# Performance work log

Measured on AMD Instinct MI355X. Metric: run time of the kernel, lower is better.

## Reference

```python
import jax, jax.numpy as jnp
import numpy as np

B, S, D, H, HS = 2, 2048, 1024, 16, 64


def setup_inputs() -> dict:
    key = jax.random.key(0)
    ks = jax.random.split(key, 4)
    x = jax.random.normal(ks[0], (B, S, D), dtype=jnp.float32)
    # causal mask: 1.0 where key_pos <= query_pos, else 0.0
    mask = jnp.tril(jnp.ones((S, S), dtype=jnp.float32))
    w_qkv = jax.random.normal(ks[1], (D, 3, H, HS), dtype=jnp.float32) * 0.02
    b_qkv = jnp.zeros((3, H, HS), dtype=jnp.float32)
    w_proj = jax.random.normal(ks[2], (H, HS, D), dtype=jnp.float32) * 0.02
    b_proj = jnp.zeros((D,), dtype=jnp.float32)
    return {"x": x, "mask": mask, "w_qkv": w_qkv, "b_qkv": b_qkv,
            "w_proj": w_proj, "b_proj": b_proj}


def reference(x, mask, w_qkv, b_qkv, w_proj, b_proj):
    # c_attn: [B,S,D] @ [D,3,H,HS] -> [B,S,3,H,HS]
    qkv = jnp.einsum('bsd,dthc->bsthc', x, w_qkv) + b_qkv
    q, k, v = qkv[:, :, 0], qkv[:, :, 1], qkv[:, :, 2]  # [B,S,H,HS]
    scale = jax.lax.rsqrt(float(HS))
    q = q * scale
    # scores over head_size: [B,H,S(query),S(key)]
    scores = jnp.einsum('bqhc,bkhc->bhqk', q, k)
    scores = scores + (1.0 - mask) * -1e9
    weights = jax.nn.softmax(scores, axis=-1).astype(x.dtype)
    # attn_pdrop = 0.0 / inference: dropout is identity
    attn = jnp.einsum('bhqk,bkhc->bqhc', weights, v)  # [B,S,H,HS]
    out = jnp.einsum('bqhc,hcd->bqd', attn, w_proj) + b_proj
    return out
```

## Files before the change

### kernel.cpp

```cpp
#include <hip/hip_runtime.h>
#include <hip/hip_bf16.h>


#define Bb 2
#define Ss 2048
#define Dd 1024
#define Hh 16
#define HSs 64

typedef __bf16 bf16x8 __attribute__((ext_vector_type(8)));
typedef float  f32x4  __attribute__((ext_vector_type(4)));

__device__ __forceinline__ unsigned short f2bf(float f) {
  unsigned int u = __float_as_uint(f);
  unsigned int lsb = (u >> 16) & 1u;
  u += 0x7fffu + lsb;
  return (unsigned short)(u >> 16);
}

__device__ __forceinline__ void async16(const unsigned short* g, unsigned short* l) {
  __builtin_amdgcn_global_load_lds(
      (const __attribute__((address_space(1))) unsigned int*)g,
      (__attribute__((address_space(3))) unsigned int*)l,
      16, 0, 0);
}

__global__ __launch_bounds__(256) void k_cvt_bf16(const float* __restrict__ in,
                                                  unsigned short* __restrict__ out,
                                                  int n) {
  int i = (blockIdx.x * 256 + threadIdx.x) * 4;
  int stride = gridDim.x * 256 * 4;
  for (; i < n; i += stride) {
    float4 v = *reinterpret_cast<const float4*>(in + i);
    ushort4 o;
    o.x = f2bf(v.x); o.y = f2bf(v.y); o.z = f2bf(v.z); o.w = f2bf(v.w);
    *reinterpret_cast<ushort4*>(out + i) = o;
  }
}

__global__ __launch_bounds__(256) void k_transpose_bf16(const float* __restrict__ in,
                                                        unsigned short* __restrict__ out,
                                                        int R, int C) {
  __shared__ float t[32][33];
  int c0 = blockIdx.x * 32, r0 = blockIdx.y * 32;
  int tx = threadIdx.x, ty = threadIdx.y;
  #pragma unroll
  for (int i = 0; i < 32; i += 8)
    t[ty + i][tx] = in[(size_t)(r0 + ty + i) * C + (c0 + tx)];
  __syncthreads();
  #pragma unroll
  for (int i = 0; i < 32; i += 8)
    out[(size_t)(c0 + ty + i) * R + (r0 + tx)] = f2bf(t[tx][ty + i]);
}

__global__ __launch_bounds__(256) void k_gemm_qkv(const unsigned short* __restrict__ A,
                                                  const unsigned short* __restrict__ Bt,
                                                  const float* __restrict__ bias,
                                                  unsigned short* __restrict__ Qg,
                                                  unsigned short* __restrict__ Kg,
                                                  unsigned short* __restrict__ Vt) {
  __shared__ unsigned short As[128 * 64];
  __shared__ unsigned short Bs[128 * 64];
  const int K = 1024;
  int bid = blockIdx.x;
  int swz = (bid % 8) * 96 + bid / 8;
  int tm = swz / 24, tn = swz % 24;
  int m0 = tm * 128, n0 = tn * 128;
  int tid = threadIdx.x;
  int w = tid >> 6, l = tid & 63;
  int lr = l & 15, lg = l >> 4;
  int wm = (w >> 1) * 64, wn = (w & 1) * 64;
  int srow = l >> 3, scol = (l & 7) * 8;

  f32x4 acc[4][4];
  #pragma unroll
  for (int i = 0; i < 4; ++i)
    #pragma unroll
    for (int j = 0; j < 4; ++j)
      acc[i][j] = (f32x4){0.f, 0.f, 0.f, 0.f};

  for (int k0 = 0; k0 < K; k0 += 64) {
    #pragma unroll
    for (int c = 0; c < 4; ++c) {
      int chunk = w * 4 + c;
      int row = chunk * 8 + srow;
      async16(&A[(size_t)(m0 + row) * K + k0 + scol], &As[chunk * 512]);
      async16(&Bt[(size_t)(n0 + row) * K + k0 + scol], &Bs[chunk * 512]);
    }
    __syncthreads();
    #pragma unroll
    for (int kk = 0; kk < 64; kk += 32) {
      bf16x8 af[4], bfr[4];
      #pragma unroll
      for (int mf = 0; mf < 4; ++mf)
        af[mf] = *reinterpret_cast<const bf16x8*>(&As[(wm + mf * 16 + lr) * 64 + kk + lg * 8]);
      #pragma unroll
      for (int nf = 0; nf < 4; ++nf)
        bfr[nf] = *reinterpret_cast<const bf16x8*>(&Bs[(wn + nf * 16 + lr) * 64 + kk + lg * 8]);
      #pragma unroll
      for (int mf = 0; mf < 4; ++mf)
        #pragma unroll
        for (int nf = 0; nf < 4; ++nf)
          acc[mf][nf] = __builtin_amdgcn_mfma_f32_16x16x32_bf16(af[mf], bfr[nf], acc[mf][nf], 0, 0, 0);
    }
    __syncthreads();
  }

  #pragma unroll
  for (int mf = 0; mf < 4; ++mf) {
    #pragma unroll
    for (int nf = 0; nf < 4; ++nf) {
      int n = n0 + wn + nf * 16 + lr;
      int t = n >> 10, r = n & 1023;
      int h = r >> 6, cc = r & 63;
      float bv = bias[n];
      if (t == 2) {
        int m = m0 + wm + mf * 16 + lg * 4;
        int b = m >> 11, s = m & 2047;
        ushort4 pk;
        pk.x = f2bf(acc[mf][nf][0] + bv);
        pk.y = f2bf(acc[mf][nf][1] + bv);
        pk.z = f2bf(acc[mf][nf][2] + bv);
        pk.w = f2bf(acc[mf][nf][3] + bv);
        *reinterpret_cast<ushort4*>(&Vt[((size_t)(b * Hh + h) * HSs + cc) * Ss + s]) = pk;
      } else {
        #pragma unroll
        for (int j = 0; j < 4; ++j) {
          int m = m0 + wm + mf * 16 + lg * 4 + j;
          int b = m >> 11, s = m & 2047;
          size_t idx = ((size_t)(b * Hh + h) * Ss + s) * HSs + cc;
          float v = acc[mf][nf][j] + bv;
          if (t == 0) Qg[idx] = f2bf(v * 0.1803368801111244f);
          else        Kg[idx] = f2bf(v);
        }
      }
    }
  }
}

__global__ __launch_bounds__(512, 4) void k_attn(const unsigned short* __restrict__ Qg,
                                                 const unsigned short* __restrict__ Kg,
                                                 const unsigned short* __restrict__ Vt,
                                                 unsigned short* __restrict__ Ob) {
  __shared__ unsigned short Ks[2][64 * 64];
  __shared__ unsigned short Vs[2][64 * 64];
  __shared__ unsigned short Ps[8][16 * 72];

  int bid = blockIdx.x;
  int pi = bid >> 5, bh = bid & 31;
  int Q = (pi < 8) ? pi : 23 - pi;
  int b = bh >> 4, h = bh & 15;
  int qs0 = Q * 128;

  int tid = threadIdx.x;
  int w = tid >> 6, l = tid & 63;
  int lr = l & 15, lg = l >> 4;
  int qw = qs0 + w * 16;
  int srow = l >> 3, scol = (l & 7) * 8;
  int swcol = scol ^ (srow << 3);
  int row = w * 8 + srow;

  bf16x8 qf[2];
  #pragma unroll
  for (int kx = 0; kx < 2; ++kx)
    qf[kx] = *reinterpret_cast<const bf16x8*>(
        &Qg[((size_t)bh * Ss + qw + lr) * HSs + kx * 32 + lg * 8]);

  f32x4 oacc[4];
  #pragma unroll
  for (int nf = 0; nf < 4; ++nf) oacc[nf] = (f32x4){0.f, 0.f, 0.f, 0.f};
  float mrun[4], lrun[4];
  #pragma unroll
  for (int j = 0; j < 4; ++j) { mrun[j] = -1e30f; lrun[j] = 0.f; }

  int ntiles = 2 * Q + 2;
  async16(&Kg[((size_t)bh * Ss + row) * HSs + swcol], &Ks[0][w * 512]);
  async16(&Vt[((size_t)bh * HSs + row) * Ss + swcol], &Vs[0][w * 512]);
  __syncthreads();

  for (int t = 0; t < ntiles; ++t) {
    int cur = t & 1;
    if (t + 1 < ntiles) {
      async16(&Kg[((size_t)bh * Ss + (t + 1) * 64 + row) * HSs + swcol], &Ks[cur ^ 1][w * 512]);
      async16(&Vt[((size_t)bh * HSs + row) * Ss + (t + 1) * 64 + swcol], &Vs[cur ^ 1][w * 512]);
    }

    if (t * 64 <= qw + 15) {
      f32x4 sacc[4];
      #pragma unroll
      for (int nf = 0; nf < 4; ++nf) sacc[nf] = (f32x4){0.f, 0.f, 0.f, 0.f};
      __builtin_amdgcn_s_setprio(1);
      #pragma unroll
      for (int kx = 0; kx < 2; ++kx) {
        bf16x8 kf[4];
        #pragma unroll
        for (int nf = 0; nf < 4; ++nf)
          kf[nf] = *reinterpret_cast<const bf16x8*>(
              &Ks[cur][(nf * 16 + lr) * 64 + ((kx * 32 + lg * 8) ^ ((lr & 7) << 3))]);
        #pragma unroll
        for (int nf = 0; nf < 4; ++nf)
          sacc[nf] = __builtin_amdgcn_mfma_f32_16x16x32_bf16(qf[kx], kf[nf], sacc[nf], 0, 0, 0);
      }
      __builtin_amdgcn_s_setprio(0);

      if (t * 64 + 63 > qw) {
        #pragma unroll
        for (int nf = 0; nf < 4; ++nf) {
          int kcol = t * 64 + nf * 16 + lr;
          #pragma unroll
          for (int j = 0; j < 4; ++j) {
            int qg2 = qw + lg * 4 + j;
            if (kcol > qg2) sacc[nf][j] = -1e30f;
          }
        }
      }

      float rmax[4];
      #pragma unroll
      for (int j = 0; j < 4; ++j) {
        float rm = fmaxf(fmaxf(sacc[0][j], sacc[1][j]), fmaxf(sacc[2][j], sacc[3][j]));
        #pragma unroll
        for (int d = 1; d < 16; d <<= 1)
          rm = fmaxf(rm, __shfl_xor(rm, d));
        rmax[j] = rm;
      }
      bool need = (rmax[0] > mrun[0] + 8.f) | (rmax[1] > mrun[1] + 8.f) |
                  (rmax[2] > mrun[2] + 8.f) | (rmax[3] > mrun[3] + 8.f);
      if (__any(need)) {
        #pragma unroll
        for (int j = 0; j < 4; ++j) {
          float mnew = fmaxf(mrun[j], rmax[j]);
          float cf = exp2f(mrun[j] - mnew);
          mrun[j] = mnew;
          lrun[j] *= cf;
          #pragma unroll
          for (int nf = 0; nf < 4; ++nf)
            oacc[nf][j] *= cf;
        }
      }
      #pragma unroll
      for (int j = 0; j < 4; ++j) {
        float psum = 0.f;
        #pragma unroll
        for (int nf = 0; nf < 4; ++nf) {
          float pv = exp2f(sacc[nf][j] - mrun[j]);
          sacc[nf][j] = pv;
          psum += pv;
        }
        #pragma unroll
        for (int d = 1; d < 16; d <<= 1)
          psum += __shfl_xor(psum, d);
        lrun[j] += psum;
      }

      #pragma unroll
      for (int nf = 0; nf < 4; ++nf)
        #pragma unroll
        for (int j = 0; j < 4; ++j)
          Ps[w][(lg * 4 + j) * 72 + nf * 16 + lr] = f2bf(sacc[nf][j]);

      __builtin_amdgcn_s_setprio(1);
      #pragma unroll
      for (int kx = 0; kx < 2; ++kx) {
        bf16x8 pf = *reinterpret_cast<const bf16x8*>(&Ps[w][lr * 72 + kx * 32 + lg * 8]);
        bf16x8 vf[4];
        #pragma unroll
        for (int nf = 0; nf < 4; ++nf)
          vf[nf] = *reinterpret_cast<const bf16x8*>(
              &Vs[cur][(nf * 16 + lr) * 64 + ((kx * 32 + lg * 8) ^ ((lr & 7) << 3))]);
        #pragma unroll
        for (int nf = 0; nf < 4; ++nf)
          oacc[nf] = __builtin_amdgcn_mfma_f32_16x16x32_bf16(pf, vf[nf], oacc[nf], 0, 0, 0);
      }
      __builtin_amdgcn_s_setprio(0);
    }
    __syncthreads();
  }

  #pragma unroll
  for (int j = 0; j < 4; ++j) {
    float rinv = 1.0f / lrun[j];
    int s = qw + lg * 4 + j;
    #pragma unroll
    for (int nf = 0; nf < 4; ++nf) {
      int c = nf * 16 + lr;
      Ob[((size_t)(b * Ss + s)) * Dd + h * HSs + c] = f2bf(oacc[nf][j] * rinv);
    }
  }
}

__global__ __launch_bounds__(256) void k_gemm_out(const unsigned short* __restrict__ A,
                                                  const unsigned short* __restrict__ Bt,
                                                  const float* __restrict__ bias,
                                                  float* __restrict__ Out) {
  __shared__ unsigned short As[128 * 64];
  __shared__ unsigned short Bs[128 * 64];
  const int K = 1024;
  int bid = blockIdx.x;
  int swz = (bid % 8) * 32 + bid / 8;
  int tm = swz / 8, tn = swz % 8;
  int m0 = tm * 128, n0 = tn * 128;
  int tid = threadIdx.x;
  int w = tid >> 6, l = tid & 63;
  int lr = l & 15, lg = l >> 4;
  int wm = (w >> 1) * 64, wn = (w & 1) * 64;
  int srow = l >> 3, scol = (l & 7) * 8;

  f32x4 acc[4][4];
  #pragma unroll
  for (int i = 0; i < 4; ++i)
    #pragma unroll
    for (int j = 0; j < 4; ++j)
      acc[i][j] = (f32x4){0.f, 0.f, 0.f, 0.f};

  for (int k0 = 0; k0 < K; k0 += 64) {
    #pragma unroll
    for (int c = 0; c < 4; ++c) {
      int chunk = w * 4 + c;
      int row = chunk * 8 + srow;
      async16(&A[(size_t)(m0 + row) * K + k0 + scol], &As[chunk * 512]);
      async16(&Bt[(size_t)(n0 + row) * K + k0 + scol], &Bs[chunk * 512]);
    }
    __syncthreads();
    #pragma unroll
    for (int kk = 0; kk < 64; kk += 32) {
      bf16x8 af[4], bfr[4];
      #pragma unroll
      for (int mf = 0; mf < 4; ++mf)
        af[mf] = *reinterpret_cast<const bf16x8*>(&As[(wm + mf * 16 + lr) * 64 + kk + lg * 8]);
      #pragma unroll
      for (int nf = 0; nf < 4; ++nf)
        bfr[nf] = *reinterpret_cast<const bf16x8*>(&Bs[(wn + nf * 16 + lr) * 64 + kk + lg * 8]);
      #pragma unroll
      for (int mf = 0; mf < 4; ++mf)
        #pragma unroll
        for (int nf = 0; nf < 4; ++nf)
          acc[mf][nf] = __builtin_amdgcn_mfma_f32_16x16x32_bf16(af[mf], bfr[nf], acc[mf][nf], 0, 0, 0);
    }
    __syncthreads();
  }

  #pragma unroll
  for (int mf = 0; mf < 4; ++mf)
    #pragma unroll
    for (int nf = 0; nf < 4; ++nf) {
      int n = n0 + wn + nf * 16 + lr;
      float bv = bias[n];
      #pragma unroll
      for (int j = 0; j < 4; ++j) {
        int m = m0 + wm + mf * 16 + lg * 4 + j;
        Out[(size_t)m * 1024 + n] = acc[mf][nf][j] + bv;
      }
    }
}

extern "C" void kernel_launch(void* const* d_in, const int* in_sizes, int n_in,
                              void* d_out, int out_size, void* d_ws, size_t ws_size,
                              hipStream_t stream) {
  (void)in_sizes; (void)n_in; (void)out_size; (void)ws_size;
  const float* x      = (const float*)d_in[0];
  const float* w_qkv  = (const float*)d_in[2];
  const float* b_qkv  = (const float*)d_in[3];
  const float* w_proj = (const float*)d_in[4];
  const float* b_proj = (const float*)d_in[5];
  float* out = (float*)d_out;

  char* ws = (char*)d_ws;
  unsigned short* xb    = (unsigned short*)(ws);
  unsigned short* wqkvT = (unsigned short*)(ws + 8388608);
  unsigned short* wpT   = (unsigned short*)(ws + 14680064);
  unsigned short* Qg    = (unsigned short*)(ws + 16777216);
  unsigned short* Kg    = (unsigned short*)(ws + 25165824);
  unsigned short* Vt    = (unsigned short*)(ws + 33554432);
  unsigned short* attnb = (unsigned short*)(ws + 41943040);

  k_cvt_bf16<<<dim3(2048), dim3(256), 0, stream>>>(x, xb, Bb * Ss * Dd);
  k_transpose_bf16<<<dim3(96, 32), dim3(32, 8), 0, stream>>>(w_qkv, wqkvT, 1024, 3072);
  k_transpose_bf16<<<dim3(32, 32), dim3(32, 8), 0, stream>>>(w_proj, wpT, 1024, 1024);
  k_gemm_qkv<<<dim3(32 * 24), dim3(256), 0, stream>>>(xb, wqkvT, b_qkv, Qg, Kg, Vt);
  k_attn<<<dim3(512), dim3(512), 0, stream>>>(Qg, Kg, Vt, attnb);
  k_gemm_out<<<dim3(32 * 8), dim3(256), 0, stream>>>(attnb, wpT, b_proj, out);
}
```

Measured before the change: 250.8 us.

## Double-buffer GEMM tiles and retile attention to 64-row query blocks

Both projection GEMMs now double-buffer their LDS tiles, prefetching the next K slice asynchronously while the current one is consumed, so there is one barrier per step instead of two. The attention kernel shrinks to 256 threads and 64-query tiles with 1024 blocks, uses a four-way zigzag mapping of query tiles for causal load balance, drops the per-wave causal skip and the setprio hints, and swizzles the P scratch buffer instead of padding it. Double buffering doubles GEMM shared memory, which may reduce occupancy, and the smaller attention tiles reload K/V more often.

```diff
diff --git a/kernel.cpp b/kernel.cpp
--- a/kernel.cpp
+++ b/kernel.cpp
@@ -59,8 +59,8 @@
                                                   unsigned short* __restrict__ Qg,
                                                   unsigned short* __restrict__ Kg,
                                                   unsigned short* __restrict__ Vt) {
-  __shared__ unsigned short As[128 * 64];
-  __shared__ unsigned short Bs[128 * 64];
+  __shared__ unsigned short As[2][128 * 64];
+  __shared__ unsigned short Bs[2][128 * 64];
   const int K = 1024;
   int bid = blockIdx.x;
   int swz = (bid % 8) * 96 + bid / 8;
@@ -79,24 +79,36 @@
     for (int j = 0; j < 4; ++j)
       acc[i][j] = (f32x4){0.f, 0.f, 0.f, 0.f};
 
-  for (int k0 = 0; k0 < K; k0 += 64) {
-    #pragma unroll
-    for (int c = 0; c < 4; ++c) {
-      int chunk = w * 4 + c;
-      int row = chunk * 8 + srow;
-      async16(&A[(size_t)(m0 + row) * K + k0 + scol], &As[chunk * 512]);
-      async16(&Bt[(size_t)(n0 + row) * K + k0 + scol], &Bs[chunk * 512]);
-    }
-    __syncthreads();
+  #pragma unroll
+  for (int c = 0; c < 4; ++c) {
+    int chunk = w * 4 + c;
+    int row = chunk * 8 + srow;
+    async16(&A[(size_t)(m0 + row) * K + scol], &As[0][chunk * 512]);
+    async16(&Bt[(size_t)(n0 + row) * K + scol], &Bs[0][chunk * 512]);
+  }
+  __syncthreads();
+
+  for (int kt = 0; kt < 16; ++kt) {
+    int cur = kt & 1;
+    if (kt < 15) {
+      int k0n = (kt + 1) * 64;
+      #pragma unroll
+      for (int c = 0; c < 4; ++c) {
+        int chunk = w * 4 + c;
+        int row = chunk * 8 + srow;
+        async16(&A[(size_t)(m0 + row) * K + k0n + scol], &As[cur ^ 1][chunk * 512]);
+        async16(&Bt[(size_t)(n0 + row) * K + k0n + scol], &Bs[cur ^ 1][chunk * 512]);
+      }
+    }
     #pragma unroll
     for (int kk = 0; kk < 64; kk += 32) {
       bf16x8 af[4], bfr[4];
       #pragma unroll
       for (int mf = 0; mf < 4; ++mf)
-        af[mf] = *reinterpret_cast<const bf16x8*>(&As[(wm + mf * 16 + lr) * 64 + kk + lg * 8]);
-      #pragma unroll
-      for (int nf = 0; nf < 4; ++nf)
-        bfr[nf] = *reinterpret_cast<const bf16x8*>(&Bs[(wn + nf * 16 + lr) * 64 + kk + lg * 8]);
+        af[mf] = *reinterpret_cast<const bf16x8*>(&As[cur][(wm + mf * 16 + lr) * 64 + kk + lg * 8]);
+      #pragma unroll
+      for (int nf = 0; nf < 4; ++nf)
+        bfr[nf] = *reinterpret_cast<const bf16x8*>(&Bs[cur][(wn + nf * 16 + lr) * 64 + kk + lg * 8]);
       #pragma unroll
       for (int mf = 0; mf < 4; ++mf)
         #pragma unroll
@@ -138,19 +150,20 @@
   }
 }
 
-__global__ __launch_bounds__(512, 4) void k_attn(const unsigned short* __restrict__ Qg,
+__global__ __launch_bounds__(256, 4) void k_attn(const unsigned short* __restrict__ Qg,
                                                  const unsigned short* __restrict__ Kg,
                                                  const unsigned short* __restrict__ Vt,
                                                  unsigned short* __restrict__ Ob) {
   __shared__ unsigned short Ks[2][64 * 64];
   __shared__ unsigned short Vs[2][64 * 64];
-  __shared__ unsigned short Ps[8][16 * 72];
+  __shared__ unsigned short Ps[4][16 * 64];
 
   int bid = blockIdx.x;
-  int pi = bid >> 5, bh = bid & 31;
-  int Q = (pi < 8) ? pi : 23 - pi;
+  int c = bid >> 8, r = bid & 255;
+  int p = r >> 5, bh = r & 31;
+  int qt = (c == 0) ? p : (c == 1) ? 15 - p : (c == 2) ? 16 + p : 31 - p;
   int b = bh >> 4, h = bh & 15;
-  int qs0 = Q * 128;
+  int qs0 = qt * 64;
 
   int tid = threadIdx.x;
   int w = tid >> 6, l = tid & 63;
@@ -158,7 +171,6 @@
   int qw = qs0 + w * 16;
   int srow = l >> 3, scol = (l & 7) * 8;
   int swcol = scol ^ (srow << 3);
-  int row = w * 8 + srow;
 
   bf16x8 qf[2];
   #pragma unroll
@@ -173,106 +185,113 @@
   #pragma unroll
   for (int j = 0; j < 4; ++j) { mrun[j] = -1e30f; lrun[j] = 0.f; }
 
-  int ntiles = 2 * Q + 2;
-  async16(&Kg[((size_t)bh * Ss + row) * HSs + swcol], &Ks[0][w * 512]);
-  async16(&Vt[((size_t)bh * HSs + row) * Ss + swcol], &Vs[0][w * 512]);
+  int ntiles = qt + 1;
+  #pragma unroll
+  for (int cch = 0; cch < 2; ++cch) {
+    int rr = w * 16 + cch * 8 + srow;
+    async16(&Kg[((size_t)bh * Ss + rr) * HSs + swcol], &Ks[0][(w * 2 + cch) * 512]);
+    async16(&Vt[((size_t)bh * HSs + rr) * Ss + swcol], &Vs[0][(w * 2 + cch) * 512]);
+  }
   __syncthreads();
 
   for (int t = 0; t < ntiles; ++t) {
     int cur = t & 1;
     if (t + 1 < ntiles) {
-      async16(&Kg[((size_t)bh * Ss + (t + 1) * 64 + row) * HSs + swcol], &Ks[cur ^ 1][w * 512]);
-      async16(&Vt[((size_t)bh * HSs + row) * Ss + (t + 1) * 64 + swcol], &Vs[cur ^ 1][w * 512]);
-    }
-
-    if (t * 64 <= qw + 15) {
-      f32x4 sacc[4];
-      #pragma unroll
-      for (int nf = 0; nf < 4; ++nf) sacc[nf] = (f32x4){0.f, 0.f, 0.f, 0.f};
-      __builtin_amdgcn_s_setprio(1);
-      #pragma unroll
-      for (int kx = 0; kx < 2; ++kx) {
-        bf16x8 kf[4];
+      #pragma unroll
+      for (int cch = 0; cch < 2; ++cch) {
+        int rr = w * 16 + cch * 8 + srow;
+        async16(&Kg[((size_t)bh * Ss + (t + 1) * 64 + rr) * HSs + swcol],
+                &Ks[cur ^ 1][(w * 2 + cch) * 512]);
+        async16(&Vt[((size_t)bh * HSs + rr) * Ss + (t + 1) * 64 + swcol],
+                &Vs[cur ^ 1][(w * 2 + cch) * 512]);
+      }
+    }
+
+    f32x4 sacc[4];
+    #pragma unroll
+    for (int nf = 0; nf < 4; ++nf) sacc[nf] = (f32x4){0.f, 0.f, 0.f, 0.f};
+    #pragma unroll
+    for (int kx = 0; kx < 2; ++kx) {
+      bf16x8 kf[4];
+      #pragma unroll
+      for (int nf = 0; nf < 4; ++nf)
+        kf[nf] = *reinterpret_cast<const bf16x8*>(
+            &Ks[cur][(nf * 16 + lr) * 64 + ((kx * 32 + lg * 8) ^ ((lr & 7) << 3))]);
+      #pragma unroll
+      for (int nf = 0; nf < 4; ++nf)
+        sacc[nf] = __builtin_amdgcn_mfma_f32_16x16x32_bf16(qf[kx], kf[nf], sacc[nf], 0, 0, 0);
+    }
+
+    if (t == qt) {
+      #pragma unroll
+      for (int nf = 0; nf < 4; ++nf) {
+        int kcol = t * 64 + nf * 16 + lr;
+        #pragma unroll
+        for (int j = 0; j < 4; ++j) {
+          int qg2 = qw + lg * 4 + j;
+          if (kcol > qg2) sacc[nf][j] = -1e30f;
+        }
+      }
+    }
+
+    float rmax[4];
+    #pragma unroll
+    for (int j = 0; j < 4; ++j) {
+      float rm = fmaxf(fmaxf(sacc[0][j], sacc[1][j]), fmaxf(sacc[2][j], sacc[3][j]));
+      #pragma unroll
+      for (int d = 1; d < 16; d <<= 1)
+        rm = fmaxf(rm, __shfl_xor(rm, d));
+      rmax[j] = rm;
+    }
+    bool need = (rmax[0] > mrun[0] + 8.f) | (rmax[1] > mrun[1] + 8.f) |
+                (rmax[2] > mrun[2] + 8.f) | (rmax[3] > mrun[3] + 8.f);
+    if (__any(need)) {
+      #pragma unroll
+      for (int j = 0; j < 4; ++j) {
+        float mnew = fmaxf(mrun[j], rmax[j]);
+        float cf = exp2f(mrun[j] - mnew);
+        mrun[j] = mnew;
+        lrun[j] *= cf;
         #pragma unroll
         for (int nf = 0; nf < 4; ++nf)
-          kf[nf] = *reinterpret_cast<const bf16x8*>(
-              &Ks[cur][(nf * 16 + lr) * 64 + ((kx * 32 + lg * 8) ^ ((lr & 7) << 3))]);
-        #pragma unroll
-        for (int nf = 0; nf < 4; ++nf)
-          sacc[nf] = __builtin_amdgcn_mfma_f32_16x16x32_bf16(qf[kx], kf[nf], sacc[nf], 0, 0, 0);
-      }
-      __builtin_amdgcn_s_setprio(0);
-
-      if (t * 64 + 63 > qw) {
-        #pragma unroll
-        for (int nf = 0; nf < 4; ++nf) {
-          int kcol = t * 64 + nf * 16 + lr;
-          #pragma unroll
-          for (int j = 0; j < 4; ++j) {
-            int qg2 = qw + lg * 4 + j;
-            if (kcol > qg2) sacc[nf][j] = -1e30f;
-          }
-        }
-      }
-
-      float rmax[4];
+          oacc[nf][j] *= cf;
+      }
+    }
+    #pragma unroll
+    for (int j = 0; j < 4; ++j) {
+      float psum = 0.f;
+      #pragma unroll
+      for (int nf = 0; nf < 4; ++nf) {
+        float pv = exp2f(sacc[nf][j] - mrun[j]);
+        sacc[nf][j] = pv;
+        psum += pv;
+      }
+      #pragma unroll
+      for (int d = 1; d < 16; d <<= 1)
+        psum += __shfl_xor(psum, d);
+      lrun[j] += psum;
+    }
+
+    #pragma unroll
+    for (int nf = 0; nf < 4; ++nf)
       #pragma unroll
       for (int j = 0; j < 4; ++j) {
-        float rm = fmaxf(fmaxf(sacc[0][j], sacc[1][j]), fmaxf(sacc[2][j], sacc[3][j]));
-        #pragma unroll
-        for (int d = 1; d < 16; d <<= 1)
-          rm = fmaxf(rm, __shfl_xor(rm, d));
-        rmax[j] = rm;
-      }
-      bool need = (rmax[0] > mrun[0] + 8.f) | (rmax[1] > mrun[1] + 8.f) |
-                  (rmax[2] > mrun[2] + 8.f) | (rmax[3] > mrun[3] + 8.f);
-      if (__any(need)) {
-        #pragma unroll
-        for (int j = 0; j < 4; ++j) {
-          float mnew = fmaxf(mrun[j], rmax[j]);
-          float cf = exp2f(mrun[j] - mnew);
-          mrun[j] = mnew;
-          lrun[j] *= cf;
-          #pragma unroll
-          for (int nf = 0; nf < 4; ++nf)
-            oacc[nf][j] *= cf;
-        }
-      }
-      #pragma unroll
-      for (int j = 0; j < 4; ++j) {
-        float psum = 0.f;
-        #pragma unroll
-        for (int nf = 0; nf < 4; ++nf) {
-          float pv = exp2f(sacc[nf][j] - mrun[j]);
-          sacc[nf][j] = pv;
-          psum += pv;
-        }
-        #pragma unroll
-        for (int d = 1; d < 16; d <<= 1)
-          psum += __shfl_xor(psum, d);
-        lrun[j] += psum;
-      }
-
-      #pragma unroll
-      for (int nf = 0; nf < 4; ++nf)
-        #pragma unroll
-        for (int j = 0; j < 4; ++j)
-          Ps[w][(lg * 4 + j) * 72 + nf * 16 + lr] = f2bf(sacc[nf][j]);
-
-      __builtin_amdgcn_s_setprio(1);
-      #pragma unroll
-      for (int kx = 0; kx < 2; ++kx) {
-        bf16x8 pf = *reinterpret_cast<const bf16x8*>(&Ps[w][lr * 72 + kx * 32 + lg * 8]);
-        bf16x8 vf[4];
-        #pragma unroll
-        for (int nf = 0; nf < 4; ++nf)
-          vf[nf] = *reinterpret_cast<const bf16x8*>(
-              &Vs[cur][(nf * 16 + lr) * 64 + ((kx * 32 + lg * 8) ^ ((lr & 7) << 3))]);
-        #pragma unroll
-        for (int nf = 0; nf < 4; ++nf)
-          oacc[nf] = __builtin_amdgcn_mfma_f32_16x16x32_bf16(pf, vf[nf], oacc[nf], 0, 0, 0);
-      }
-      __builtin_amdgcn_s_setprio(0);
+        int prow = lg * 4 + j;
+        Ps[w][prow * 64 + ((nf * 16 + lr) ^ ((prow & 7) << 3))] = f2bf(sacc[nf][j]);
+      }
+
+    #pragma unroll
+    for (int kx = 0; kx < 2; ++kx) {
+      bf16x8 pf = *reinterpret_cast<const bf16x8*>(
+          &Ps[w][lr * 64 + ((kx * 32 + lg * 8) ^ ((lr & 7) << 3))]);
+      bf16x8 vf[4];
+      #pragma unroll
+      for (int nf = 0; nf < 4; ++nf)
+        vf[nf] = *reinterpret_cast<const bf16x8*>(
+            &Vs[cur][(nf * 16 + lr) * 64 + ((kx * 32 + lg * 8) ^ ((lr & 7) << 3))]);
+      #pragma unroll
+      for (int nf = 0; nf < 4; ++nf)
+        oacc[nf] = __builtin_amdgcn_mfma_f32_16x16x32_bf16(pf, vf[nf], oacc[nf], 0, 0, 0);
     }
     __syncthreads();
   }
@@ -283,8 +302,8 @@
     int s = qw + lg * 4 + j;
     #pragma unroll
     for (int nf = 0; nf < 4; ++nf) {
-      int c = nf * 16 + lr;
-      Ob[((size_t)(b * Ss + s)) * Dd + h * HSs + c] = f2bf(oacc[nf][j] * rinv);
+      int cc = nf * 16 + lr;
+      Ob[((size_t)(b * Ss + s)) * Dd + h * HSs + cc] = f2bf(oacc[nf][j] * rinv);
     }
   }
 }
@@ -293,8 +312,8 @@
                                                   const unsigned short* __restrict__ Bt,
                                                   const float* __restrict__ bias,
                                                   float* __restrict__ Out) {
-  __shared__ unsigned short As[128 * 64];
-  __shared__ unsigned short Bs[128 * 64];
+  __shared__ unsigned short As[2][128 * 64];
+  __shared__ unsigned short Bs[2][128 * 64];
   const int K = 1024;
   int bid = blockIdx.x;
   int swz = (bid % 8) * 32 + bid / 8;
@@ -313,24 +332,36 @@
     for (int j = 0; j < 4; ++j)
       acc[i][j] = (f32x4){0.f, 0.f, 0.f, 0.f};
 
-  for (int k0 = 0; k0 < K; k0 += 64) {
-    #pragma unroll
-    for (int c = 0; c < 4; ++c) {
-      int chunk = w * 4 + c;
-      int row = chunk * 8 + srow;
-      async16(&A[(size_t)(m0 + row) * K + k0 + scol], &As[chunk * 512]);
-      async16(&Bt[(size_t)(n0 + row) * K + k0 + scol], &Bs[chunk * 512]);
-    }
-    __syncthreads();
+  #pragma unroll
+  for (int c = 0; c < 4; ++c) {
+    int chunk = w * 4 + c;
+    int row = chunk * 8 + srow;
+    async16(&A[(size_t)(m0 + row) * K + scol], &As[0][chunk * 512]);
+    async16(&Bt[(size_t)(n0 + row) * K + scol], &Bs[0][chunk * 512]);
+  }
+  __syncthreads();
+
+  for (int kt = 0; kt < 16; ++kt) {
+    int cur = kt & 1;
+    if (kt < 15) {
+      int k0n = (kt + 1) * 64;
+      #pragma unroll
+      for (int c = 0; c < 4; ++c) {
+        int chunk = w * 4 + c;
+        int row = chunk * 8 + srow;
+        async16(&A[(size_t)(m0 + row) * K + k0n + scol], &As[cur ^ 1][chunk * 512]);
+        async16(&Bt[(size_t)(n0 + row) * K + k0n + scol], &Bs[cur ^ 1][chunk * 512]);
+      }
+    }
     #pragma unroll
     for (int kk = 0; kk < 64; kk += 32) {
       bf16x8 af[4], bfr[4];
       #pragma unroll
       for (int mf = 0; mf < 4; ++mf)
-        af[mf] = *reinterpret_cast<const bf16x8*>(&As[(wm + mf * 16 + lr) * 64 + kk + lg * 8]);
-      #pragma unroll
-      for (int nf = 0; nf < 4; ++nf)
-        bfr[nf] = *reinterpret_cast<const bf16x8*>(&Bs[(wn + nf * 16 + lr) * 64 + kk + lg * 8]);
+        af[mf] = *reinterpret_cast<const bf16x8*>(&As[cur][(wm + mf * 16 + lr) * 64 + kk + lg * 8]);
+      #pragma unroll
+      for (int nf = 0; nf < 4; ++nf)
+        bfr[nf] = *reinterpret_cast<const bf16x8*>(&Bs[cur][(wn + nf * 16 + lr) * 64 + kk + lg * 8]);
       #pragma unroll
       for (int mf = 0; mf < 4; ++mf)
         #pragma unroll
@@ -378,6 +409,6 @@
   k_transpose_bf16<<<dim3(96, 32), dim3(32, 8), 0, stream>>>(w_qkv, wqkvT, 1024, 3072);
   k_transpose_bf16<<<dim3(32, 32), dim3(32, 8), 0, stream>>>(w_proj, wpT, 1024, 1024);
   k_gemm_qkv<<<dim3(32 * 24), dim3(256), 0, stream>>>(xb, wqkvT, b_qkv, Qg, Kg, Vt);
-  k_attn<<<dim3(512), dim3(512), 0, stream>>>(Qg, Kg, Vt, attnb);
+  k_attn<<<dim3(1024), dim3(256), 0, stream>>>(Qg, Kg, Vt, attnb);
   k_gemm_out<<<dim3(32 * 8), dim3(256), 0, stream>>>(attnb, wpT, b_proj, out);
 }
```

After: 259.2 us. 3.4% more time.
